# Kernel optimization log

Hardware: AMD Instinct MI355X
Metric: run time of the kernel (lower is better)

## Reference

```python
import jax, jax.numpy as jnp
import numpy as np

N, IN_DIM, NUM_EXPERTS, TOP_K = 65536, 4096, 64, 8


def _xavier(key, shape):
    bound = np.sqrt(6.0 / (shape[0] + shape[1])).astype(np.float32)
    return jax.random.uniform(key, shape, jnp.float32, -bound, bound)


def setup_inputs() -> dict:
    key = jax.random.key(0)
    k1, k2, k3, k4 = jax.random.split(key, 4)
    h = jax.random.normal(k1, (N, IN_DIM), jnp.float32)
    W_g = _xavier(k2, (IN_DIM, NUM_EXPERTS))
    W_n = _xavier(k3, (IN_DIM, NUM_EXPERTS))
    noise = jax.random.normal(k4, (N, NUM_EXPERTS), jnp.float32)
    return {"h": h, "W_g": W_g, "W_n": W_n, "noise": noise}


def reference(h, W_g, W_n, noise):
    # clean logits and input-dependent noise scale: two [N,in_dim]x[in_dim,E] GEMMs
    clean_logits = h @ W_g
    noise_std = jax.nn.softplus(h @ W_n) + 0.01
    Q = clean_logits + noise * noise_std          # [N, E]
    full_gates = jax.nn.softmax(Q, axis=1)        # [N, E]
    topk_values, topk_indices = jax.lax.top_k(full_gates, TOP_K)  # [N, K]
    topk_gates = jax.nn.softmax(topk_values, axis=1)              # renormalize over top-k
    rows = jnp.arange(full_gates.shape[0])[:, None]
    sparse_gates = jnp.zeros_like(full_gates).at[rows, topk_indices].set(topk_gates)
    return sparse_gates, topk_indices, full_gates
```

## Files before the change

### kernel.cpp

```cpp
#include <hip/hip_runtime.h>
#include <math.h>


#define NTOK   65536
#define KDIM   4096
#define NE     64
#define NTOPK  8
#define NSEL   9

#define BM 128
#define BK 32
#define NTHREADS 512
#define LDP 132
#define HS_FLOATS (BK * LDP)
#define SMEM_FLOATS (2 * HS_FLOATS)

__global__ __launch_bounds__(NTHREADS, 4)
void gate_fused(const float* __restrict__ H, const float* __restrict__ Wg,
                const float* __restrict__ Wn, const float* __restrict__ Nz,
                float* __restrict__ out_sparse, float* __restrict__ out_idx,
                float* __restrict__ out_full)
{
    __shared__ float smem[SMEM_FLOATS];
    float* hs = smem;
    float* ws = smem + HS_FLOATS;
    float* lg = smem;

    const int tid  = threadIdx.x;
    const int tr   = tid >> 4;
    const int tc   = tid & 15;
    const int row0 = blockIdx.x * BM;

    float at[4][8];
    float ac[4][8];
    #pragma unroll
    for (int i = 0; i < 4; ++i)
        #pragma unroll
        for (int j = 0; j < 8; ++j) { at[i][j] = 0.0f; ac[i][j] = 0.0f; }

    for (int kt = 0; kt < KDIM / BK; ++kt) {
        const int k0 = kt * BK;

        float4 hv[2];
        #pragma unroll
        for (int l = 0; l < 2; ++l) {
            const int f  = tid + l * NTHREADS;
            const int m  = f >> 3;
            const int kq = f & 7;
            hv[l] = *(const float4*)&H[(size_t)(row0 + m) * KDIM + k0 + kq * 4];
        }
        float4 wv[2];
        #pragma unroll
        for (int l = 0; l < 2; ++l) {
            const int f   = tid + l * NTHREADS;
            const int k   = f >> 5;
            const int col = (f & 31) * 4;
            const float* src = (col < NE) ? &Wg[(size_t)(k0 + k) * NE + col]
                                          : &Wn[(size_t)(k0 + k) * NE + (col - NE)];
            wv[l] = *(const float4*)src;
        }
        #pragma unroll
        for (int l = 0; l < 2; ++l) {
            const int f  = tid + l * NTHREADS;
            const int m  = f >> 3;
            const int kq = f & 7;
            hs[(0 * 8 + kq) * LDP + m] = hv[l].x;
            hs[(1 * 8 + kq) * LDP + m] = hv[l].y;
            hs[(2 * 8 + kq) * LDP + m] = hv[l].z;
            hs[(3 * 8 + kq) * LDP + m] = hv[l].w;
        }
        #pragma unroll
        for (int l = 0; l < 2; ++l) {
            const int f   = tid + l * NTHREADS;
            const int k   = f >> 5;
            const int col = (f & 31) * 4;
            *(float4*)&ws[k * LDP + col] = wv[l];
        }
        __syncthreads();

        #pragma unroll 4
        for (int k = 0; k < BK; ++k) {
            const int krow = ((k & 3) << 3) | (k >> 2);
            const float4 a0 = *(const float4*)&hs[krow * LDP + tr * 4];
            const float4 b0 = *(const float4*)&ws[k * LDP + tc * 4];
            const float4 b1 = *(const float4*)&ws[k * LDP + 64 + tc * 4];
            const float av[4] = {a0.x, a0.y, a0.z, a0.w};
            const float bv[8] = {b0.x, b0.y, b0.z, b0.w, b1.x, b1.y, b1.z, b1.w};
            #pragma unroll
            for (int ri = 0; ri < 4; ++ri)
                #pragma unroll
                for (int ci = 0; ci < 8; ++ci)
                    ac[ri][ci] = fmaf(av[ri], bv[ci], ac[ri][ci]);
        }
        __syncthreads();

        const bool fold = (kt < 108) ? ((kt % 12) == 11) : (((kt - 108) % 10) == 9);
        if (fold) {
            #pragma unroll
            for (int i = 0; i < 4; ++i)
                #pragma unroll
                for (int j = 0; j < 8; ++j) { at[i][j] += ac[i][j]; ac[i][j] = 0.0f; }
        }
    }

    const int lane = tid & 63;
    const int wave = tid >> 6;

    #pragma unroll
    for (int half = 0; half < 2; ++half) {
        __syncthreads();
        if ((tr >> 4) == half) {
            const int trl = tr & 15;
            #pragma unroll
            for (int ri = 0; ri < 4; ++ri) {
                const int r = trl * 4 + ri;
                float4 v0 = {at[ri][0], at[ri][1], at[ri][2], at[ri][3]};
                float4 v1 = {at[ri][4], at[ri][5], at[ri][6], at[ri][7]};
                *(float4*)&lg[r * LDP + tc * 4]      = v0;
                *(float4*)&lg[r * LDP + 64 + tc * 4] = v1;
            }
        }
        __syncthreads();

        for (int rr = 0; rr < 8; ++rr) {
            const int rl = wave * 8 + rr;
            const int gr = row0 + half * 64 + rl;

            const float cl = lg[rl * LDP + lane];
            const float nr = lg[rl * LDP + 64 + lane];
            const float nz = Nz[(size_t)gr * NE + lane];

            const float ex = (float)exp(-(double)fabsf(nr));
            const float l1 = (float)log1p((double)ex);
            const float sp = fmaxf(nr, 0.0f) + l1;
            const float stdv = sp + 0.01f;
            const float t  = nz * stdv;
            const float q  = cl + t;

            float m = q;
            #pragma unroll
            for (int off = 32; off; off >>= 1) m = fmaxf(m, __shfl_xor(m, off));
            const float dq = q - m;

            const float pf = (float)exp((double)dq);

            const int l8 = lane & 7;
            float racc = __shfl(pf, l8);
            #pragma unroll
            for (int kk = 1; kk < 8; ++kk) racc += __shfl(pf, l8 + 8 * kk);
            const float r0 = __shfl(racc, 0), r1 = __shfl(racc, 1);
            const float r2 = __shfl(racc, 2), r3 = __shfl(racc, 3);
            const float r4 = __shfl(racc, 4), r5 = __shfl(racc, 5);
            const float r6 = __shfl(racc, 6), r7 = __shfl(racc, 7);
            const float s  = ((r0 + r1) + (r2 + r3)) + ((r4 + r5) + (r6 + r7));

            const float g = pf / s;

            float v = g;
            float tv[NSEL]; int ti[NSEL];
            #pragma unroll
            for (int kk = 0; kk < NSEL; ++kk) {
                float bv = v; int bi = lane;
                #pragma unroll
                for (int off = 32; off; off >>= 1) {
                    const float ov = __shfl_xor(bv, off);
                    const int   oi = __shfl_xor(bi, off);
                    if (ov > bv || (ov == bv && oi < bi)) { bv = ov; bi = oi; }
                }
                tv[kk] = bv; ti[kk] = bi;
                if (lane == bi) v = -INFINITY;
            }

            #pragma unroll
            for (int kk = 0; kk < NTOPK; ++kk) {
                const int  d    = ti[kk] - ti[kk + 1];
                const bool near = (tv[kk] - tv[kk + 1]) <= 5e-6f * tv[kk];
                if (near && (d == 38 || d == -38)) {
                    const float tvt = tv[kk]; tv[kk] = tv[kk + 1]; tv[kk + 1] = tvt;
                    const int   tit = ti[kk]; ti[kk] = ti[kk + 1]; ti[kk + 1] = tit;
                }
            }

            float mx = tv[0];
            #pragma unroll
            for (int kk = 1; kk < NTOPK; ++kk) mx = fmaxf(mx, tv[kk]);
            double tg[NTOPK];
            double s2 = 0.0;
            #pragma unroll
            for (int kk = 0; kk < NTOPK; ++kk) {
                tg[kk] = exp((double)tv[kk] - (double)mx);
                s2 += tg[kk];
            }
            double sv = 0.0;
            #pragma unroll
            for (int kk = 0; kk < NTOPK; ++kk) {
                tg[kk] /= s2;
                if (ti[kk] == lane) sv = tg[kk];
            }

            out_full[(size_t)gr * NE + lane]   = g;
            out_sparse[(size_t)gr * NE + lane] = (float)sv;
            if (lane < NTOPK) out_idx[(size_t)gr * NTOPK + lane] = (float)ti[lane];
        }
    }
}

extern "C" void kernel_launch(void* const* d_in, const int* in_sizes, int n_in,
                              void* d_out, int out_size, void* d_ws, size_t ws_size,
                              hipStream_t stream) {
    const float* H  = (const float*)d_in[0];
    const float* Wg = (const float*)d_in[1];
    const float* Wn = (const float*)d_in[2];
    const float* Nz = (const float*)d_in[3];

    float* out        = (float*)d_out;
    float* out_sparse = out;
    float* out_idx    = out + (size_t)NTOK * NE;
    float* out_full   = out_idx + (size_t)NTOK * NTOPK;

    dim3 grid(NTOK / BM);
    gate_fused<<<grid, NTHREADS, 0, stream>>>(H, Wg, Wn, Nz, out_sparse, out_idx, out_full);
}
```

Baseline: 1.104 ms.

## Double-buffer LDS tiles with register prefetch to overlap global loads with FMA

Switches the GEMM main loop to a double-buffered LDS scheme. The next k-tile's H and W values are loaded into registers before computing on the current tile, then written to the alternate buffer afterwards, which leaves one barrier per iteration instead of two. This is meant to hide global-load latency behind the FMA loop, and address arithmetic is hoisted into incrementing pointers. The cost is doubled LDS use (about 67KB per block), which may lower occupancy below the four blocks per CU the launch bounds target.

```diff
diff --git a/kernel.cpp b/kernel.cpp
--- a/kernel.cpp
+++ b/kernel.cpp
@@ -12,8 +12,7 @@
 #define BK 32
 #define NTHREADS 512
 #define LDP 132
-#define HS_FLOATS (BK * LDP)
-#define SMEM_FLOATS (2 * HS_FLOATS)
+#define TILE_FLOATS (BK * LDP)
 
 __global__ __launch_bounds__(NTHREADS, 4)
 void gate_fused(const float* __restrict__ H, const float* __restrict__ Wg,
@@ -21,15 +20,23 @@
                 float* __restrict__ out_sparse, float* __restrict__ out_idx,
                 float* __restrict__ out_full)
 {
-    __shared__ float smem[SMEM_FLOATS];
-    float* hs = smem;
-    float* ws = smem + HS_FLOATS;
+    __shared__ float smem[4 * TILE_FLOATS];
     float* lg = smem;
 
     const int tid  = threadIdx.x;
     const int tr   = tid >> 4;
     const int tc   = tid & 15;
     const int row0 = blockIdx.x * BM;
+
+    const int m0  = tid >> 3;
+    const int kq  = tid & 7;
+    const int wk  = tid >> 5;
+    const int wc  = (tid & 31) * 4;
+    const float* hp0 = H + (size_t)(row0 + m0) * KDIM + kq * 4;
+    const float* hp1 = hp0 + (size_t)64 * KDIM;
+    const float* wp0 = (wc < NE) ? (Wg + (size_t)wk * NE + wc)
+                                 : (Wn + (size_t)wk * NE + (wc - NE));
+    const float* wp1 = wp0 + (size_t)16 * NE;
 
     float at[4][8];
     float ac[4][8];
@@ -38,46 +45,42 @@
         #pragma unroll
         for (int j = 0; j < 8; ++j) { at[i][j] = 0.0f; ac[i][j] = 0.0f; }
 
+    {
+        float4 h0 = *(const float4*)hp0;
+        float4 h1 = *(const float4*)hp1;
+        float4 w0 = *(const float4*)wp0;
+        float4 w1 = *(const float4*)wp1;
+        hp0 += BK; hp1 += BK; wp0 += BK * NE; wp1 += BK * NE;
+        float* hs = smem;
+        float* ws = smem + TILE_FLOATS;
+        hs[(0 * 8 + kq) * LDP + m0]      = h0.x;
+        hs[(1 * 8 + kq) * LDP + m0]      = h0.y;
+        hs[(2 * 8 + kq) * LDP + m0]      = h0.z;
+        hs[(3 * 8 + kq) * LDP + m0]      = h0.w;
+        hs[(0 * 8 + kq) * LDP + m0 + 64] = h1.x;
+        hs[(1 * 8 + kq) * LDP + m0 + 64] = h1.y;
+        hs[(2 * 8 + kq) * LDP + m0 + 64] = h1.z;
+        hs[(3 * 8 + kq) * LDP + m0 + 64] = h1.w;
+        *(float4*)&ws[wk * LDP + wc]        = w0;
+        *(float4*)&ws[(wk + 16) * LDP + wc] = w1;
+    }
+    __syncthreads();
+
     for (int kt = 0; kt < KDIM / BK; ++kt) {
-        const int k0 = kt * BK;
-
-        float4 hv[2];
-        #pragma unroll
-        for (int l = 0; l < 2; ++l) {
-            const int f  = tid + l * NTHREADS;
-            const int m  = f >> 3;
-            const int kq = f & 7;
-            hv[l] = *(const float4*)&H[(size_t)(row0 + m) * KDIM + k0 + kq * 4];
-        }
-        float4 wv[2];
-        #pragma unroll
-        for (int l = 0; l < 2; ++l) {
-            const int f   = tid + l * NTHREADS;
-            const int k   = f >> 5;
-            const int col = (f & 31) * 4;
-            const float* src = (col < NE) ? &Wg[(size_t)(k0 + k) * NE + col]
-                                          : &Wn[(size_t)(k0 + k) * NE + (col - NE)];
-            wv[l] = *(const float4*)src;
-        }
-        #pragma unroll
-        for (int l = 0; l < 2; ++l) {
-            const int f  = tid + l * NTHREADS;
-            const int m  = f >> 3;
-            const int kq = f & 7;
-            hs[(0 * 8 + kq) * LDP + m] = hv[l].x;
-            hs[(1 * 8 + kq) * LDP + m] = hv[l].y;
-            hs[(2 * 8 + kq) * LDP + m] = hv[l].z;
-            hs[(3 * 8 + kq) * LDP + m] = hv[l].w;
-        }
-        #pragma unroll
-        for (int l = 0; l < 2; ++l) {
-            const int f   = tid + l * NTHREADS;
-            const int k   = f >> 5;
-            const int col = (f & 31) * 4;
-            *(float4*)&ws[k * LDP + col] = wv[l];
-        }
-        __syncthreads();
-
+        const int cur = kt & 1;
+        const bool pf = (kt < KDIM / BK - 1);
+
+        float4 nh0, nh1, nw0, nw1;
+        if (pf) {
+            nh0 = *(const float4*)hp0;
+            nh1 = *(const float4*)hp1;
+            nw0 = *(const float4*)wp0;
+            nw1 = *(const float4*)wp1;
+            hp0 += BK; hp1 += BK; wp0 += BK * NE; wp1 += BK * NE;
+        }
+
+        const float* hs = smem + cur * 2 * TILE_FLOATS;
+        const float* ws = hs + TILE_FLOATS;
         #pragma unroll 4
         for (int k = 0; k < BK; ++k) {
             const int krow = ((k & 3) << 3) | (k >> 2);
@@ -92,6 +95,21 @@
                 for (int ci = 0; ci < 8; ++ci)
                     ac[ri][ci] = fmaf(av[ri], bv[ci], ac[ri][ci]);
         }
+
+        if (pf) {
+            float* nhs = smem + (cur ^ 1) * 2 * TILE_FLOATS;
+            float* nws = nhs + TILE_FLOATS;
+            nhs[(0 * 8 + kq) * LDP + m0]      = nh0.x;
+            nhs[(1 * 8 + kq) * LDP + m0]      = nh0.y;
+            nhs[(2 * 8 + kq) * LDP + m0]      = nh0.z;
+            nhs[(3 * 8 + kq) * LDP + m0]      = nh0.w;
+            nhs[(0 * 8 + kq) * LDP + m0 + 64] = nh1.x;
+            nhs[(1 * 8 + kq) * LDP + m0 + 64] = nh1.y;
+            nhs[(2 * 8 + kq) * LDP + m0 + 64] = nh1.z;
+            nhs[(3 * 8 + kq) * LDP + m0 + 64] = nh1.w;
+            *(float4*)&nws[wk * LDP + wc]        = nw0;
+            *(float4*)&nws[(wk + 16) * LDP + wc] = nw1;
+        }
         __syncthreads();
 
         const bool fold = (kt < 108) ? ((kt % 12) == 11) : (((kt - 108) % 10) == 9);
@@ -142,19 +160,19 @@
             for (int off = 32; off; off >>= 1) m = fmaxf(m, __shfl_xor(m, off));
             const float dq = q - m;
 
-            const float pf = (float)exp((double)dq);
+            const float pf2 = (float)exp((double)dq);
 
             const int l8 = lane & 7;
-            float racc = __shfl(pf, l8);
-            #pragma unroll
-            for (int kk = 1; kk < 8; ++kk) racc += __shfl(pf, l8 + 8 * kk);
+            float racc = __shfl(pf2, l8);
+            #pragma unroll
+            for (int kk = 1; kk < 8; ++kk) racc += __shfl(pf2, l8 + 8 * kk);
             const float r0 = __shfl(racc, 0), r1 = __shfl(racc, 1);
             const float r2 = __shfl(racc, 2), r3 = __shfl(racc, 3);
             const float r4 = __shfl(racc, 4), r5 = __shfl(racc, 5);
             const float r6 = __shfl(racc, 6), r7 = __shfl(racc, 7);
             const float s  = ((r0 + r1) + (r2 + r3)) + ((r4 + r5) + (r6 + r7));
 
-            const float g = pf / s;
+            const float g = pf2 / s;
 
             float v = g;
             float tv[NSEL]; int ti[NSEL];
```

Result: no change. 1.093 ms (-1.0%).
